# Optimization experiments

Hardware: AMD Instinct MI355X
Metric: run time of the kernel (lower is better)

The kernel has to match this reference:

```python
import jax, jax.numpy as jnp
import numpy as np

EPS = 1e-6
BLK = 64          # VSA coarse block size
H = 12            # num attention heads


def _ln(x, w=None, b=None):
    m = jnp.mean(x, -1, keepdims=True)
    v = jnp.mean((x - m) ** 2, -1, keepdims=True)
    y = (x - m) * jax.lax.rsqrt(v + EPS)
    return y * w + b if w is not None else y


def _rms(x, w):
    return x * jax.lax.rsqrt(jnp.mean(x * x, -1, keepdims=True) + EPS) * w


def _rope(x, cos, sin):
    # non-neox (interleaved) rotary; x: [B,S,H,D], cos/sin: [S,D/2]
    x1, x2 = x[..., 0::2], x[..., 1::2]
    c, s = cos[None, :, None, :], sin[None, :, None, :]
    return jnp.stack([x1 * c - x2 * s, x2 * c + x1 * s], -1).reshape(x.shape)


def _attn(q, k, v):
    scale = 1.0 / np.sqrt(q.shape[-1])
    p = jax.nn.softmax(jnp.einsum('bshd,bthd->bhst', q, k) * scale, -1)
    return jnp.einsum('bhst,bthd->bshd', p, v)


def setup_inputs() -> dict:
    key = jax.random.key(0)
    ks = jax.random.split(key, 24)
    B, S, L2, DIM, FFN = 1, 2048, 512, 1536, 8960
    D = DIM // H
    # rope tables
    pos = jnp.arange(S, dtype=jnp.float32)
    inv = 1.0 / (10000.0 ** (jnp.arange(D // 2, dtype=jnp.float32) / (D // 2)))
    ang = pos[:, None] * inv[None, :]
    w = lambda k, shape, fan: jax.random.normal(k, shape, jnp.float32) / np.sqrt(fan)
    return {
        'hidden_states': jax.random.normal(ks[0], (B, S, DIM), jnp.float32),
        'encoder_hidden_states': jax.random.normal(ks[1], (B, L2, DIM), jnp.float32),
        'temb': jax.random.normal(ks[2], (B, 6, DIM), jnp.float32),
        'rope_cos': jnp.cos(ang), 'rope_sin': jnp.sin(ang),
        'scale_shift_table': w(ks[3], (1, 6, DIM), DIM),
        'Wq': w(ks[4], (DIM, DIM), DIM), 'bq': jnp.zeros((DIM,), jnp.float32),
        'Wk': w(ks[5], (DIM, DIM), DIM), 'bk': jnp.zeros((DIM,), jnp.float32),
        'Wv': w(ks[6], (DIM, DIM), DIM), 'bv': jnp.zeros((DIM,), jnp.float32),
        'Wg': w(ks[7], (DIM, DIM), DIM), 'bg': jnp.zeros((DIM,), jnp.float32),
        'Wo': w(ks[8], (DIM, DIM), DIM), 'bo': jnp.zeros((DIM,), jnp.float32),
        'nq_w': jnp.ones((DIM,), jnp.float32), 'nk_w': jnp.ones((DIM,), jnp.float32),
        'saln_w': jnp.ones((DIM,), jnp.float32), 'saln_b': jnp.zeros((DIM,), jnp.float32),
        'cWq': w(ks[9], (DIM, DIM), DIM), 'cbq': jnp.zeros((DIM,), jnp.float32),
        'cWk': w(ks[10], (DIM, DIM), DIM), 'cbk': jnp.zeros((DIM,), jnp.float32),
        'cWv': w(ks[11], (DIM, DIM), DIM), 'cbv': jnp.zeros((DIM,), jnp.float32),
        'cWo': w(ks[12], (DIM, DIM), DIM), 'cbo': jnp.zeros((DIM,), jnp.float32),
        'cnq_w': jnp.ones((DIM,), jnp.float32), 'cnk_w': jnp.ones((DIM,), jnp.float32),
        'W1': w(ks[13], (DIM, FFN), DIM), 'b1': jnp.zeros((FFN,), jnp.float32),
        'W2': w(ks[14], (FFN, DIM), FFN), 'b2': jnp.zeros((DIM,), jnp.float32),
    }


def reference(hidden_states, encoder_hidden_states, temb, rope_cos, rope_sin,
              scale_shift_table, Wq, bq, Wk, bk, Wv, bv, Wg, bg, Wo, bo,
              nq_w, nk_w, saln_w, saln_b,
              cWq, cbq, cWk, cbk, cWv, cbv, cWo, cbo, cnq_w, cnk_w,
              W1, b1, W2, b2):
    B, S, DIM = hidden_states.shape
    D = DIM // H
    # AdaLN modulation
    e = scale_shift_table + temb  # [B,6,DIM]
    shift, scale, gate, c_shift, c_scale, c_gate = [e[:, i:i + 1] for i in range(6)]
    x = hidden_states
    n = _ln(x) * (1.0 + scale) + shift
    # QKV + gate_compress projections, RMSNorm across heads on q/k
    q = _rms(n @ Wq + bq, nq_w).reshape(B, S, H, D)
    k = _rms(n @ Wk + bk, nk_w).reshape(B, S, H, D)
    v = (n @ Wv + bv).reshape(B, S, H, D)
    g = (n @ Wg + bg).reshape(B, S, H, D)
    q = _rope(q, rope_cos, rope_sin)
    k = _rope(k, rope_cos, rope_sin)
    # VSA: fine (dense, all blocks selected) + gated coarse (block-mean-pooled)
    fine = _attn(q, k, v)
    Nb = S // BLK
    qc = q.reshape(B, Nb, BLK, H, D).mean(2)
    kc = k.reshape(B, Nb, BLK, H, D).mean(2)
    vc = v.reshape(B, Nb, BLK, H, D).mean(2)
    coarse = jnp.repeat(_attn(qc, kc, vc), BLK, axis=1)  # [B,S,H,D]
    ao = (fine + coarse * g).reshape(B, S, DIM) @ Wo + bo
    # self-attn residual + affine LN (null shift/scale)
    hidden = x + gate * ao
    n2 = _ln(hidden, saln_w, saln_b)
    # T2V cross attention
    cq = _rms(n2 @ cWq + cbq, cnq_w).reshape(B, S, H, D)
    ck = _rms(encoder_hidden_states @ cWk + cbk, cnk_w).reshape(B, -1, H, D)
    cv = (encoder_hidden_states @ cWv + cbv).reshape(B, -1, H, D)
    co = _attn(cq, ck, cv).reshape(B, S, DIM) @ cWo + cbo
    hidden = hidden + co
    n3 = _ln(hidden) * (1.0 + c_scale) + c_shift
    # FFN with tanh-approx GELU, gated residual
    ffn = jax.nn.gelu(n3 @ W1 + b1, approximate=True) @ W2 + b2
    return hidden + c_gate * ffn
```

## Files before the change

kernel.cpp:

```cpp
#include <hip/hip_runtime.h>

#define DIMH 1536
#define NH 12
#define DH 128
#define SQ 2048
#define SKV 512
#define FFNH 8960

typedef short short8v __attribute__((ext_vector_type(8)));
typedef short short4v __attribute__((ext_vector_type(4)));
typedef float f32x4 __attribute__((ext_vector_type(4)));

union U8 { unsigned short u[8]; short8v v; };
union U4 { unsigned short u[4]; short4v v; };

__device__ __forceinline__ unsigned short f2bf(float f) {
  unsigned int u = __float_as_uint(f);
  u += 0x7fffu + ((u >> 16) & 1u);
  return (unsigned short)(u >> 16);
}
__device__ __forceinline__ float bf2f(unsigned short u) {
  return __uint_as_float((unsigned int)u << 16);
}

__device__ __forceinline__ void gld16(const void* g, void* l) {
  __builtin_amdgcn_global_load_lds(
      (const __attribute__((address_space(1))) unsigned int*)g,
      (__attribute__((address_space(3))) unsigned int*)l, 16, 0, 0);
}


__global__ void prep_e(const float* __restrict__ sst, const float* __restrict__ temb,
                       float* __restrict__ e) {
  int i = blockIdx.x * 256 + threadIdx.x;
  if (i < 6 * DIMH) e[i] = sst[i] + temb[i];
}

__global__ void concat4(const float* __restrict__ a, const float* __restrict__ b,
                        const float* __restrict__ c, const float* __restrict__ d,
                        float* __restrict__ o) {
  int i = blockIdx.x * 256 + threadIdx.x;
  int which = i / DIMH, r = i - which * DIMH;
  float v;
  if (which == 0) v = a[r];
  else if (which == 1) v = b[r];
  else if (which == 2) v = c[r];
  else v = d[r];
  o[i] = v;
}

__global__ void cast_f32_bf16(const float* __restrict__ x, unsigned short* __restrict__ y,
                              int n) {
  int i = blockIdx.x * 256 + threadIdx.x;
  if (i < n) y[i] = f2bf(x[i]);
}

__global__ __launch_bounds__(256) void transpose_bf16(const float* __restrict__ W,
    unsigned short* __restrict__ Wt, int K, int N) {
  __shared__ float T[32][33];
  int n0 = blockIdx.x * 32, k0 = blockIdx.y * 32;
  int tx = threadIdx.x & 31, ty = threadIdx.x >> 5;
#pragma unroll
  for (int p = 0; p < 4; p++)
    T[ty + p * 8][tx] = W[(long)(k0 + ty + p * 8) * N + n0 + tx];
  __syncthreads();
#pragma unroll
  for (int p = 0; p < 4; p++)
    Wt[(long)(n0 + ty + p * 8) * K + k0 + tx] = f2bf(T[tx][ty + p * 8]);
}

__global__ __launch_bounds__(256) void vtrans(const unsigned short* __restrict__ v, int vs,
    unsigned short* __restrict__ vt, int S) {
  __shared__ unsigned short T[32][33];
  int s0 = blockIdx.x * 32, c0 = blockIdx.y * 32;
  int tx = threadIdx.x & 31, ty = threadIdx.x >> 5;
#pragma unroll
  for (int p = 0; p < 4; p++)
    T[ty + p * 8][tx] = v[(long)(s0 + ty + p * 8) * vs + c0 + tx];
  __syncthreads();
  int head = c0 / DH, dbase = c0 - head * DH;
#pragma unroll
  for (int p = 0; p < 4; p++)
    vt[(long)head * DH * S + (long)(dbase + ty + p * 8) * S + s0 + tx] = T[tx][ty + p * 8];
}

__device__ __forceinline__ float blockReduceSum(float val) {
  __shared__ float sm[4];
#pragma unroll
  for (int off = 32; off > 0; off >>= 1) val += __shfl_xor(val, off, 64);
  if ((threadIdx.x & 63) == 0) sm[threadIdx.x >> 6] = val;
  __syncthreads();
  val = sm[0] + sm[1] + sm[2] + sm[3];
  __syncthreads();
  return val;
}

__global__ __launch_bounds__(256) void layernorm_affine(const float* __restrict__ x,
    unsigned short* __restrict__ out, const float* __restrict__ g,
    const float* __restrict__ b, float add1) {
  long row = blockIdx.x;
  int tid = threadIdx.x;
  const float* xr = x + row * DIMH;
  float v[6];
  float s = 0.f;
#pragma unroll
  for (int i = 0; i < 6; i++) { v[i] = xr[tid + i * 256]; s += v[i]; }
  s = blockReduceSum(s);
  float mean = s * (1.f / DIMH);
  float s2 = 0.f;
#pragma unroll
  for (int i = 0; i < 6; i++) { float d = v[i] - mean; s2 += d * d; }
  s2 = blockReduceSum(s2);
  float inv = rsqrtf(s2 * (1.f / DIMH) + 1e-6f);
  unsigned short* o = out + row * DIMH;
#pragma unroll
  for (int i = 0; i < 6; i++) {
    int c = tid + i * 256;
    o[c] = f2bf((v[i] - mean) * inv * (g[c] + add1) + b[c]);
  }
}

__global__ __launch_bounds__(256) void rms_rope(unsigned short* __restrict__ x, int xs,
    const float* __restrict__ w, const float* __restrict__ cosb,
    const float* __restrict__ sinb, int do_rope, float sc) {
  __shared__ float xr[DIMH];
  long row = blockIdx.x;
  int tid = threadIdx.x;
  unsigned short* xp = x + row * xs;
  float ss = 0.f;
#pragma unroll
  for (int i = 0; i < 6; i++) {
    float t = bf2f(xp[tid + i * 256]);
    xr[tid + i * 256] = t;
    ss += t * t;
  }
  ss = blockReduceSum(ss);
  float inv = rsqrtf(ss * (1.f / DIMH) + 1e-6f) * sc;
#pragma unroll
  for (int j = 0; j < 3; j++) {
    int p = tid + j * 256;
    int h = p >> 6, i = p & 63;
    int d1 = h * DH + 2 * i;
    float v1 = xr[d1] * inv * w[d1];
    float v2 = xr[d1 + 1] * inv * w[d1 + 1];
    float o1 = v1, o2 = v2;
    if (do_rope) {
      float c = cosb[row * 64 + i], s = sinb[row * 64 + i];
      o1 = v1 * c - v2 * s;
      o2 = v2 * c + v1 * s;
    }
    xp[d1] = f2bf(o1);
    xp[d1 + 1] = f2bf(o2);
  }
}

__global__ void pool64(const unsigned short* __restrict__ src, int ss,
                       float* __restrict__ dst) {
  int c = blockIdx.x * 256 + threadIdx.x;
  int nb = blockIdx.y;
  float s = 0.f;
  for (int j = 0; j < 64; j++) s += bf2f(src[(long)(nb * 64 + j) * ss + c]);
  dst[nb * DIMH + c] = s * (1.f / 64.f);
}

__global__ void combine_fine(unsigned short* __restrict__ fine,
                             const float* __restrict__ coarse,
                             const unsigned short* __restrict__ g, int gs) {
  int i = blockIdx.x * 256 + threadIdx.x;
  int srow = i / DIMH, c = i - srow * DIMH;
  fine[i] = f2bf(bf2f(fine[i]) + coarse[(srow >> 6) * DIMH + c] * bf2f(g[(long)srow * gs + c]));
}


__global__ __launch_bounds__(256) void coarse_attn(const float* __restrict__ qc,
    const float* __restrict__ kc, const float* __restrict__ vc, float* __restrict__ co) {
  __shared__ float S[32 * 33];
  int h = blockIdx.x, tid = threadIdx.x;
  for (int e = tid; e < 1024; e += 256) {
    int i = e >> 5, j = e & 31;
    float d = 0.f;
    for (int d0 = 0; d0 < DH; d0++)
      d += qc[i * DIMH + h * DH + d0] * kc[j * DIMH + h * DH + d0];
    S[i * 33 + j] = d;
  }
  __syncthreads();
  if (tid < 32) {
    float m = -3.4e38f;
    for (int j = 0; j < 32; j++) m = fmaxf(m, S[tid * 33 + j]);
    float sum = 0.f;
    for (int j = 0; j < 32; j++) {
      float p = __expf(S[tid * 33 + j] - m);
      S[tid * 33 + j] = p;
      sum += p;
    }
    float r = 1.f / sum;
    for (int j = 0; j < 32; j++) S[tid * 33 + j] *= r;
  }
  __syncthreads();
  for (int e = tid; e < 32 * DH; e += 256) {
    int i = e >> 7, d = e & 127;
    float o = 0.f;
    for (int j = 0; j < 32; j++) o += S[i * 33 + j] * vc[j * DIMH + h * DH + d];
    co[i * DIMH + h * DH + d] = o;
  }
}


#define LDP 68

__global__ __launch_bounds__(256, 3) void flash3(const unsigned short* __restrict__ Q, int qs,
    const unsigned short* __restrict__ Kx, int kstr, const unsigned short* __restrict__ Vt,
    unsigned short* __restrict__ O, int ostr, int Sk,
    float* __restrict__ ml, long zstride, int skchunk) {
  __shared__ unsigned short Ks[64 * 128];
  __shared__ unsigned short Vs[128 * 64];
  __shared__ unsigned short P[4][16 * LDP];
  int tid = threadIdx.x;
  int w = tid >> 6, lane = tid & 63;
  int quad = lane >> 4, l16 = lane & 15;
  int h = blockIdx.y, bz = blockIdx.z;
  long q0 = (long)blockIdx.x * 64 + w * 16;
  const unsigned short* Vh = Vt + (long)h * DH * Sk;
  unsigned short* Pw = P[w];

  int t_begin = bz * skchunk;
  int t_end = t_begin + skchunk;
  if (t_end > Sk) t_end = Sk;

  int rK = lane >> 4, cK = lane & 15;
  const unsigned short* KgA = Kx + (long)(w * 16 + rK) * kstr + h * DH + (cK ^ rK) * 8;
  const unsigned short* KgB = Kx + (long)(w * 16 + rK) * kstr + h * DH + ((cK ^ rK) ^ 4) * 8;
  int rV = lane >> 3, cV = lane & 7;
  const unsigned short* Vg = Vh + (long)(w * 32 + rV) * Sk + (cV ^ rV) * 8;

  short8v qf[4];
  {
    const unsigned short* qp = Q + (q0 + l16) * qs + h * DH + quad * 8;
#pragma unroll
    for (int kt = 0; kt < 4; kt++) qf[kt] = *(const short8v*)(qp + kt * 32);
  }
  float m_i = -3.4e38f, l_i = 0.f;
  f32x4 o[8];
#pragma unroll
  for (int nt = 0; nt < 8; nt++) o[nt] = (f32x4){0.f, 0.f, 0.f, 0.f};

  int kch[4];
#pragma unroll
  for (int kt = 0; kt < 4; kt++) kch[kt] = ((kt * 4 + quad) ^ (l16 & 7)) * 8;

  for (int t0 = t_begin; t0 < t_end; t0 += 64) {
    __syncthreads();
#pragma unroll
    for (int j = 0; j < 4; j++) {
      const unsigned short* ksrc = (j & 1) ? KgB : KgA;
      gld16(ksrc + (long)(t0 + j * 4) * kstr, &Ks[(w * 16 + j * 4) * 128]);
      gld16(Vg + (long)(j * 8) * Sk + t0, &Vs[(w * 32 + j * 8) * 64]);
    }
    __syncthreads();

    f32x4 sc[4];
#pragma unroll
    for (int tt = 0; tt < 4; tt++) {
      const unsigned short* kr = &Ks[(tt * 16 + l16) * 128];
      f32x4 a = (f32x4){0.f, 0.f, 0.f, 0.f};
#pragma unroll
      for (int kt = 0; kt < 4; kt++)
        a = __builtin_amdgcn_mfma_f32_16x16x32_bf16(*(const short8v*)(kr + kch[kt]),
                                                    qf[kt], a, 0, 0, 0);
      sc[tt] = a;
    }
    float mx = -3.4e38f;
#pragma unroll
    for (int tt = 0; tt < 4; tt++)
#pragma unroll
      for (int r = 0; r < 4; r++) mx = fmaxf(mx, sc[tt][r]);
    mx = fmaxf(mx, __shfl_xor(mx, 16, 64));
    mx = fmaxf(mx, __shfl_xor(mx, 32, 64));
    float mnew = fmaxf(m_i, mx);
    float rs = 0.f;
#pragma unroll
    for (int tt = 0; tt < 4; tt++) {
      U4 pk;
#pragma unroll
      for (int r = 0; r < 4; r++) {
        float pe = __expf(sc[tt][r] - mnew);
        rs += pe;
        pk.u[r] = f2bf(pe);
      }
      *(short4v*)&Pw[l16 * LDP + tt * 16 + quad * 4] = pk.v;
    }
    rs += __shfl_xor(rs, 16, 64);
    rs += __shfl_xor(rs, 32, 64);
    float alpha = __expf(m_i - mnew);
    l_i = l_i * alpha + rs;
    m_i = mnew;
    float ar[4];
#pragma unroll
    for (int r = 0; r < 4; r++) ar[r] = __shfl(alpha, quad * 4 + r, 16);
#pragma unroll
    for (int nt = 0; nt < 8; nt++) {
      f32x4 t = o[nt];
      t[0] *= ar[0]; t[1] *= ar[1]; t[2] *= ar[2]; t[3] *= ar[3];
      o[nt] = t;
    }
#pragma unroll
    for (int c = 0; c < 2; c++) {
      short8v ap = *(const short8v*)&Pw[l16 * LDP + c * 32 + quad * 8];
#pragma unroll
      for (int nt = 0; nt < 8; nt++) {
        short8v bv = *(const short8v*)&Vs[(nt * 16 + l16) * 64 +
                                          (((c * 4 + quad) ^ (l16 & 7)) * 8)];
        o[nt] = __builtin_amdgcn_mfma_f32_16x16x32_bf16(ap, bv, o[nt], 0, 0, 0);
      }
    }
  }
  if (ml) {
    if (quad == 0) {
      float* mlp = ml + ((size_t)(bz * NH + h) * SQ + q0 + l16) * 2;
      mlp[0] = m_i;
      mlp[1] = l_i;
    }
    unsigned short* Ow = O + (long)bz * zstride;
#pragma unroll
    for (int nt = 0; nt < 8; nt++)
#pragma unroll
      for (int r = 0; r < 4; r++)
        Ow[(q0 + quad * 4 + r) * ostr + h * DH + nt * 16 + l16] = f2bf(o[nt][r]);
  } else {
    float linv[4];
#pragma unroll
    for (int r = 0; r < 4; r++) linv[r] = 1.f / __shfl(l_i, quad * 4 + r, 16);
#pragma unroll
    for (int nt = 0; nt < 8; nt++)
#pragma unroll
      for (int r = 0; r < 4; r++)
        O[(q0 + quad * 4 + r) * ostr + h * DH + nt * 16 + l16] = f2bf(o[nt][r] * linv[r]);
  }
}

__global__ __launch_bounds__(192) void attn_combine(const unsigned short* __restrict__ parts,
    const float* __restrict__ ml, int nz, unsigned short* __restrict__ fine, int fstr) {
  __shared__ float wgt[4][NH];
  __shared__ float linv[NH];
  int q = blockIdx.x, tid = threadIdx.x;
  if (tid < NH) {
    float m = -3.4e38f;
    for (int z = 0; z < nz; z++)
      m = fmaxf(m, ml[((size_t)(z * NH + tid) * SQ + q) * 2]);
    float l = 0.f;
    for (int z = 0; z < nz; z++) {
      const float* p = &ml[((size_t)(z * NH + tid) * SQ + q) * 2];
      float wz = __expf(p[0] - m);
      wgt[z][tid] = wz;
      l += p[1] * wz;
    }
    linv[tid] = 1.f / l;
  }
  __syncthreads();
  int c0 = tid * 8, h = c0 >> 7;
  float acc[8];
#pragma unroll
  for (int j = 0; j < 8; j++) acc[j] = 0.f;
  for (int z = 0; z < nz; z++) {
    U8 pv;
    pv.v = *(const short8v*)&parts[(size_t)z * SQ * DIMH + (size_t)q * DIMH + c0];
    float wz = wgt[z][h];
#pragma unroll
    for (int j = 0; j < 8; j++) acc[j] += bf2f(pv.u[j]) * wz;
  }
  U8 ov;
  float li = linv[h];
#pragma unroll
  for (int j = 0; j < 8; j++) ov.u[j] = f2bf(acc[j] * li);
  *(short8v*)&fine[(size_t)q * fstr + c0] = ov.v;
}


__global__ __launch_bounds__(256) void gemm3(const unsigned short* __restrict__ A, int lda,
    const unsigned short* __restrict__ Wt, const float* __restrict__ bias,
    void* __restrict__ outv, int ldc, const float* __restrict__ res,
    const float* __restrict__ gvec, int M, int N, int K, int kchunk, int mode) {
  __shared__ unsigned short As[128 * 64];
  __shared__ unsigned short Bs[128 * 64];
  int tid = threadIdx.x;
  int m0 = blockIdx.x * 128, n0 = blockIdx.y * 128;
  int wave = tid >> 6, lane = tid & 63;
  int quad = lane >> 4, l16 = lane & 15;
  int wm = (wave & 1) * 64, wn = (wave >> 1) * 64;
  int k0 = blockIdx.z * kchunk;
  int k1 = k0 + kchunk; if (k1 > K) k1 = K;

  int rofs = lane >> 3;
  int schunk = (lane & 7) ^ rofs;
  const unsigned short* Ag = A + (long)(m0 + wave * 32 + rofs) * lda + schunk * 8;
  const unsigned short* Bg = Wt + (long)(n0 + wave * 32 + rofs) * (long)K + schunk * 8;
  unsigned short* Albase = &As[(wave * 32) * 64];
  unsigned short* Blbase = &Bs[(wave * 32) * 64];

  f32x4 acc[4][4];
#pragma unroll
  for (int mt = 0; mt < 4; mt++)
#pragma unroll
    for (int nt = 0; nt < 4; nt++) acc[mt][nt] = (f32x4){0.f, 0.f, 0.f, 0.f};

  for (int kb = k0; kb < k1; kb += 64) {
    __syncthreads();
#pragma unroll
    for (int j = 0; j < 4; j++) {
      gld16(Ag + (long)(j * 8) * lda + kb, Albase + (j * 8) * 64);
      gld16(Bg + (long)(j * 8) * K + kb, Blbase + (j * 8) * 64);
    }
    __syncthreads();
#pragma unroll
    for (int ks = 0; ks < 2; ks++) {
      short8v af[4], bfr[4];
#pragma unroll
      for (int mt = 0; mt < 4; mt++) {
        int r = wm + mt * 16 + l16;
        af[mt] = *(const short8v*)&As[r * 64 + (((ks * 4 + quad) ^ (r & 7)) * 8)];
      }
#pragma unroll
      for (int nt = 0; nt < 4; nt++) {
        int r = wn + nt * 16 + l16;
        bfr[nt] = *(const short8v*)&Bs[r * 64 + (((ks * 4 + quad) ^ (r & 7)) * 8)];
      }
#pragma unroll
      for (int mt = 0; mt < 4; mt++)
#pragma unroll
        for (int nt = 0; nt < 4; nt++)
          acc[mt][nt] = __builtin_amdgcn_mfma_f32_16x16x32_bf16(af[mt], bfr[nt], acc[mt][nt], 0, 0, 0);
    }
  }

  long zoff = (mode == 3) ? (long)blockIdx.z * M * (long)ldc : 0;
#pragma unroll
  for (int mt = 0; mt < 4; mt++)
#pragma unroll
    for (int nt = 0; nt < 4; nt++)
#pragma unroll
      for (int r = 0; r < 4; r++) {
        int row = m0 + wm + mt * 16 + quad * 4 + r;
        int col = n0 + wn + nt * 16 + l16;
        float v = acc[mt][nt][r];
        if (bias) v += bias[col];
        if (mode == 1) {
          float z = 0.7978845608028654f * (v + 0.044715f * v * v * v);
          float e2 = __expf(2.f * z);
          float th_ = 1.f - 2.f / (e2 + 1.f);
          v = 0.5f * v * (1.f + th_);
        }
        long idx = (long)row * ldc + col;
        if (mode == 2) {
          float gv = gvec ? gvec[col] : 1.f;
          ((float*)outv)[idx] = res[idx] + gv * v;
        } else {
          ((unsigned short*)outv)[zoff + idx] = f2bf(v);
        }
      }
}

__global__ void reduce_splitk(const unsigned short* __restrict__ p, int nsplit,
                              const float* __restrict__ hid, const float* __restrict__ b2,
                              const float* __restrict__ gvec, float* __restrict__ out) {
  int i = blockIdx.x * 256 + threadIdx.x;
  int c = i % DIMH;
  float s = 0.f;
  for (int z = 0; z < nsplit; z++) s += bf2f(p[(long)z * SQ * DIMH + i]);
  out[i] = hid[i] + gvec[c] * (s + b2[c]);
}


extern "C" void kernel_launch(void* const* d_in, const int* in_sizes, int n_in,
                              void* d_out, int out_size, void* d_ws, size_t ws_size,
                              hipStream_t stream) {
  (void)in_sizes; (void)n_in; (void)out_size;
  const float* hs   = (const float*)d_in[0];
  const float* enc  = (const float*)d_in[1];
  const float* temb = (const float*)d_in[2];
  const float* rc   = (const float*)d_in[3];
  const float* rsn  = (const float*)d_in[4];
  const float* sst  = (const float*)d_in[5];
  const float* Wq = (const float*)d_in[6];   const float* bq = (const float*)d_in[7];
  const float* Wk = (const float*)d_in[8];   const float* bk = (const float*)d_in[9];
  const float* Wv = (const float*)d_in[10];  const float* bv = (const float*)d_in[11];
  const float* Wg = (const float*)d_in[12];  const float* bg = (const float*)d_in[13];
  const float* Wo = (const float*)d_in[14];  const float* bo = (const float*)d_in[15];
  const float* nq_w = (const float*)d_in[16];  const float* nk_w = (const float*)d_in[17];
  const float* saln_w = (const float*)d_in[18]; const float* saln_b = (const float*)d_in[19];
  const float* cWq = (const float*)d_in[20]; const float* cbq = (const float*)d_in[21];
  const float* cWk = (const float*)d_in[22]; const float* cbk = (const float*)d_in[23];
  const float* cWv = (const float*)d_in[24]; const float* cbv = (const float*)d_in[25];
  const float* cWo = (const float*)d_in[26]; const float* cbo = (const float*)d_in[27];
  const float* cnq_w = (const float*)d_in[28]; const float* cnk_w = (const float*)d_in[29];
  const float* W1 = (const float*)d_in[30];  const float* b1 = (const float*)d_in[31];
  const float* W2 = (const float*)d_in[32];  const float* b2 = (const float*)d_in[33];
  float* outp = (float*)d_out;
  const float attn_scale = 0.08838834764831845f;

  char* base = (char*)d_ws;
  size_t off = 0;
  auto alloc = [&](size_t bytes) -> void* {
    void* p = (void*)(base + off);
    off += (bytes + 255) & ~(size_t)255;
    return p;
  };
  const long ACTE = (long)SQ * DIMH;
  float* e     = (float*)alloc(6 * DIMH * 4);
  float* bias4 = (float*)alloc(4 * DIMH * 4);
  unsigned short* nbuf = (unsigned short*)alloc(ACTE * 2);
  unsigned short* R    = (unsigned short*)alloc((size_t)SQ * FFNH * 2);
  float* hid           = (float*)alloc(ACTE * 4);
  unsigned short* WT   = (unsigned short*)alloc((size_t)FFNH * DIMH * 2);
  unsigned short* vt   = (unsigned short*)alloc((size_t)NH * DH * SQ * 2);
  unsigned short* encb = (unsigned short*)alloc((size_t)SKV * DIMH * 2);
  float* qc  = (float*)alloc(32 * DIMH * 4);
  float* kc  = (float*)alloc(32 * DIMH * 4);
  float* vc  = (float*)alloc(32 * DIMH * 4);
  float* cob = (float*)alloc(32 * DIMH * 4);
  float* mlbuf = (float*)alloc((size_t)4 * NH * SQ * 2 * 4);
  size_t fixed_off = off;
  int nsplit = 4;
  unsigned short* parts = (unsigned short*)alloc((size_t)4 * ACTE * 2);
  if (off > ws_size) { off = fixed_off; nsplit = 2; parts = (unsigned short*)alloc((size_t)2 * ACTE * 2); }
  if (off > ws_size) { nsplit = 1; }
  int asplit = (nsplit >= 2) ? 2 : 1;

  unsigned short* qkvg = R;
  unsigned short* qb   = R;
  unsigned short* kb   = R + DIMH;
  unsigned short* vb   = R + 2 * DIMH;
  unsigned short* gb   = R + 3 * DIMH;
  unsigned short* fine = R + 4 * ACTE;
  unsigned short* qb2  = R;
  unsigned short* kb2  = R + ACTE;
  unsigned short* vb2  = R + ACTE + (long)SKV * DIMH;
  unsigned short* f1   = R;

  prep_e<<<36, 256, 0, stream>>>(sst, temb, e);
  concat4<<<24, 256, 0, stream>>>(bq, bk, bv, bg, bias4);

  layernorm_affine<<<SQ, 256, 0, stream>>>(hs, nbuf, e + DIMH, e, 1.f);

  dim3 tsq(DIMH / 32, DIMH / 32);
  transpose_bf16<<<tsq, 256, 0, stream>>>(Wq, WT + 0L * DIMH * DIMH, DIMH, DIMH);
  transpose_bf16<<<tsq, 256, 0, stream>>>(Wk, WT + 1L * DIMH * DIMH, DIMH, DIMH);
  transpose_bf16<<<tsq, 256, 0, stream>>>(Wv, WT + 2L * DIMH * DIMH, DIMH, DIMH);
  transpose_bf16<<<tsq, 256, 0, stream>>>(Wg, WT + 3L * DIMH * DIMH, DIMH, DIMH);
  gemm3<<<dim3(SQ / 128, 4 * DIMH / 128), 256, 0, stream>>>(
      nbuf, DIMH, WT, bias4, qkvg, 4 * DIMH, nullptr, nullptr, SQ, 4 * DIMH, DIMH, DIMH, 0);

  rms_rope<<<SQ, 256, 0, stream>>>(qb, 4 * DIMH, nq_w, rc, rsn, 1, attn_scale);
  rms_rope<<<SQ, 256, 0, stream>>>(kb, 4 * DIMH, nk_w, rc, rsn, 1, 1.f);

  pool64<<<dim3(6, 32), 256, 0, stream>>>(qb, 4 * DIMH, qc);
  pool64<<<dim3(6, 32), 256, 0, stream>>>(kb, 4 * DIMH, kc);
  pool64<<<dim3(6, 32), 256, 0, stream>>>(vb, 4 * DIMH, vc);

  vtrans<<<dim3(SQ / 32, DIMH / 32), 256, 0, stream>>>(vb, 4 * DIMH, vt, SQ);
  if (asplit > 1) {
    flash3<<<dim3(SQ / 64, NH, asplit), 256, 0, stream>>>(qb, 4 * DIMH, kb, 4 * DIMH, vt,
        parts, DIMH, SQ, mlbuf, ACTE, SQ / asplit);
    coarse_attn<<<NH, 256, 0, stream>>>(qc, kc, vc, cob);
    attn_combine<<<SQ, 192, 0, stream>>>(parts, mlbuf, asplit, fine, DIMH);
  } else {
    flash3<<<dim3(SQ / 64, NH), 256, 0, stream>>>(qb, 4 * DIMH, kb, 4 * DIMH, vt,
                                                  fine, DIMH, SQ, nullptr, 0, SQ);
    coarse_attn<<<NH, 256, 0, stream>>>(qc, kc, vc, cob);
  }
  combine_fine<<<SQ * DIMH / 256, 256, 0, stream>>>(fine, cob, gb, 4 * DIMH);

  transpose_bf16<<<tsq, 256, 0, stream>>>(Wo, WT, DIMH, DIMH);
  gemm3<<<dim3(SQ / 128, DIMH / 128), 256, 0, stream>>>(
      fine, DIMH, WT, bo, hid, DIMH, hs, e + 2 * DIMH, SQ, DIMH, DIMH, DIMH, 2);

  layernorm_affine<<<SQ, 256, 0, stream>>>(hid, nbuf, saln_w, saln_b, 0.f);
  transpose_bf16<<<tsq, 256, 0, stream>>>(cWq, WT, DIMH, DIMH);
  gemm3<<<dim3(SQ / 128, DIMH / 128), 256, 0, stream>>>(
      nbuf, DIMH, WT, cbq, qb2, DIMH, nullptr, nullptr, SQ, DIMH, DIMH, DIMH, 0);
  rms_rope<<<SQ, 256, 0, stream>>>(qb2, DIMH, cnq_w, nullptr, nullptr, 0, attn_scale);

  cast_f32_bf16<<<SKV * DIMH / 256, 256, 0, stream>>>(enc, encb, SKV * DIMH);
  transpose_bf16<<<tsq, 256, 0, stream>>>(cWk, WT, DIMH, DIMH);
  gemm3<<<dim3(SKV / 128, DIMH / 128), 256, 0, stream>>>(
      encb, DIMH, WT, cbk, kb2, DIMH, nullptr, nullptr, SKV, DIMH, DIMH, DIMH, 0);
  transpose_bf16<<<tsq, 256, 0, stream>>>(cWv, WT, DIMH, DIMH);
  gemm3<<<dim3(SKV / 128, DIMH / 128), 256, 0, stream>>>(
      encb, DIMH, WT, cbv, vb2, DIMH, nullptr, nullptr, SKV, DIMH, DIMH, DIMH, 0);
  rms_rope<<<SKV, 256, 0, stream>>>(kb2, DIMH, cnk_w, nullptr, nullptr, 0, 1.f);

  vtrans<<<dim3(SKV / 32, DIMH / 32), 256, 0, stream>>>(vb2, DIMH, vt, SKV);
  if (asplit > 1) {
    flash3<<<dim3(SQ / 64, NH, asplit), 256, 0, stream>>>(qb2, DIMH, kb2, DIMH, vt,
        parts, DIMH, SKV, mlbuf, ACTE, SKV / asplit);
    attn_combine<<<SQ, 192, 0, stream>>>(parts, mlbuf, asplit, fine, DIMH);
  } else {
    flash3<<<dim3(SQ / 64, NH), 256, 0, stream>>>(qb2, DIMH, kb2, DIMH, vt,
                                                  fine, DIMH, SKV, nullptr, 0, SKV);
  }
  transpose_bf16<<<tsq, 256, 0, stream>>>(cWo, WT, DIMH, DIMH);
  gemm3<<<dim3(SQ / 128, DIMH / 128), 256, 0, stream>>>(
      fine, DIMH, WT, cbo, hid, DIMH, hid, nullptr, SQ, DIMH, DIMH, DIMH, 2);

  layernorm_affine<<<SQ, 256, 0, stream>>>(hid, nbuf, e + 4 * DIMH, e + 3 * DIMH, 1.f);
  transpose_bf16<<<dim3(FFNH / 32, DIMH / 32), 256, 0, stream>>>(W1, WT, DIMH, FFNH);
  gemm3<<<dim3(SQ / 128, FFNH / 128), 256, 0, stream>>>(
      nbuf, DIMH, WT, b1, f1, FFNH, nullptr, nullptr, SQ, FFNH, DIMH, DIMH, 1);
  transpose_bf16<<<dim3(DIMH / 32, FFNH / 32), 256, 0, stream>>>(W2, WT, FFNH, DIMH);
  if (nsplit == 1) {
    gemm3<<<dim3(SQ / 128, DIMH / 128), 256, 0, stream>>>(
        f1, FFNH, WT, b2, outp, DIMH, hid, e + 5 * DIMH, SQ, DIMH, FFNH, FFNH, 2);
  } else {
    gemm3<<<dim3(SQ / 128, DIMH / 128, nsplit), 256, 0, stream>>>(
        f1, FFNH, WT, nullptr, parts, DIMH, nullptr, nullptr, SQ, DIMH, FFNH, FFNH / nsplit, 3);
    reduce_splitk<<<SQ * DIMH / 256, 256, 0, stream>>>(parts, nsplit, hid, b2,
                                                       e + 5 * DIMH, outp);
  }
}
```

Baseline: 1.018 ms.

## Double-buffer GEMM LDS tiles and remap workgroups across XCDs

The main GEMM kernel now uses two LDS buffers per operand and prefetches the tile two steps ahead. It uses explicit vmcnt waits and barriers so global-to-LDS loads overlap with MFMA compute, instead of two full syncthreads per K step. Workgroup IDs are remapped so that consecutive logical tiles land on the same XCD, aiming for better L2 reuse. Launch bounds now request two blocks per CU, but the doubled LDS footprint and the register cap may limit occupancy or cause spills.

```diff
diff --git a/kernel.cpp b/kernel.cpp
--- a/kernel.cpp
+++ b/kernel.cpp
@@ -376,14 +376,21 @@
 }
 
 
-__global__ __launch_bounds__(256) void gemm3(const unsigned short* __restrict__ A, int lda,
+__global__ __launch_bounds__(256, 2) void gemm3(const unsigned short* __restrict__ A, int lda,
     const unsigned short* __restrict__ Wt, const float* __restrict__ bias,
     void* __restrict__ outv, int ldc, const float* __restrict__ res,
     const float* __restrict__ gvec, int M, int N, int K, int kchunk, int mode) {
-  __shared__ unsigned short As[128 * 64];
-  __shared__ unsigned short Bs[128 * 64];
+  __shared__ unsigned short As[2][128 * 64];
+  __shared__ unsigned short Bs[2][128 * 64];
   int tid = threadIdx.x;
-  int m0 = blockIdx.x * 128, n0 = blockIdx.y * 128;
+
+  int gx = gridDim.x, nwg = gx * gridDim.y;
+  int orig = blockIdx.y * gx + blockIdx.x;
+  int q8 = nwg >> 3, r8 = nwg & 7;
+  int xcd = orig & 7, sub = orig >> 3;
+  int logical = (xcd < r8 ? xcd * (q8 + 1) : r8 * (q8 + 1) + (xcd - r8) * q8) + sub;
+  int m0 = (logical % gx) * 128, n0 = (logical / gx) * 128;
+
   int wave = tid >> 6, lane = tid & 63;
   int quad = lane >> 4, l16 = lane & 15;
   int wm = (wave & 1) * 64, wn = (wave >> 1) * 64;
@@ -394,8 +401,6 @@
   int schunk = (lane & 7) ^ rofs;
   const unsigned short* Ag = A + (long)(m0 + wave * 32 + rofs) * lda + schunk * 8;
   const unsigned short* Bg = Wt + (long)(n0 + wave * 32 + rofs) * (long)K + schunk * 8;
-  unsigned short* Albase = &As[(wave * 32) * 64];
-  unsigned short* Blbase = &Bs[(wave * 32) * 64];
 
   f32x4 acc[4][4];
 #pragma unroll
@@ -403,32 +408,48 @@
 #pragma unroll
     for (int nt = 0; nt < 4; nt++) acc[mt][nt] = (f32x4){0.f, 0.f, 0.f, 0.f};
 
-  for (int kb = k0; kb < k1; kb += 64) {
-    __syncthreads();
+  int nk = (k1 - k0) >> 6;
+  auto stage = [&](int buf, int kb) {
 #pragma unroll
     for (int j = 0; j < 4; j++) {
-      gld16(Ag + (long)(j * 8) * lda + kb, Albase + (j * 8) * 64);
-      gld16(Bg + (long)(j * 8) * K + kb, Blbase + (j * 8) * 64);
-    }
-    __syncthreads();
+      gld16(Ag + (long)(j * 8) * lda + kb, &As[buf][(wave * 32 + j * 8) * 64]);
+      gld16(Bg + (long)(j * 8) * K + kb, &Bs[buf][(wave * 32 + j * 8) * 64]);
+    }
+  };
+  stage(0, k0);
+  if (nk > 1) stage(1, k0 + 64);
+
+  for (int t = 0; t < nk; ++t) {
+    if (t < nk - 1) asm volatile("s_waitcnt vmcnt(8)" ::: "memory");
+    else            asm volatile("s_waitcnt vmcnt(0)" ::: "memory");
+    __builtin_amdgcn_s_barrier();
+    __builtin_amdgcn_sched_barrier(0);
+    const unsigned short* Asb = As[t & 1];
+    const unsigned short* Bsb = Bs[t & 1];
 #pragma unroll
     for (int ks = 0; ks < 2; ks++) {
       short8v af[4], bfr[4];
 #pragma unroll
       for (int mt = 0; mt < 4; mt++) {
-        int r = wm + mt * 16 + l16;
-        af[mt] = *(const short8v*)&As[r * 64 + (((ks * 4 + quad) ^ (r & 7)) * 8)];
+        int rr = wm + mt * 16 + l16;
+        af[mt] = *(const short8v*)&Asb[rr * 64 + (((ks * 4 + quad) ^ (rr & 7)) * 8)];
       }
 #pragma unroll
       for (int nt = 0; nt < 4; nt++) {
-        int r = wn + nt * 16 + l16;
-        bfr[nt] = *(const short8v*)&Bs[r * 64 + (((ks * 4 + quad) ^ (r & 7)) * 8)];
+        int rr = wn + nt * 16 + l16;
+        bfr[nt] = *(const short8v*)&Bsb[rr * 64 + (((ks * 4 + quad) ^ (rr & 7)) * 8)];
       }
 #pragma unroll
       for (int mt = 0; mt < 4; mt++)
 #pragma unroll
         for (int nt = 0; nt < 4; nt++)
           acc[mt][nt] = __builtin_amdgcn_mfma_f32_16x16x32_bf16(af[mt], bfr[nt], acc[mt][nt], 0, 0, 0);
+    }
+    if (t + 2 < nk) {
+      asm volatile("s_waitcnt lgkmcnt(0)" ::: "memory");
+      __builtin_amdgcn_s_barrier();
+      __builtin_amdgcn_sched_barrier(0);
+      stage(t & 1, k0 + (t + 2) * 64);
     }
   }
 
```

After: 958.3 us. 1.06x faster.
